# Kernel tuning notes

Hardware: AMD Instinct MI355X
Metric: run time of the kernel (lower is better)

## Reference

```python
import jax, jax.numpy as jnp
import numpy as np
import math


def setup_inputs() -> dict:
    key = jax.random.key(0)
    ks = jax.random.split(key, 5)
    B, C, E = 4, 2048, 1024
    max_len = 2048
    s = 1.0 / math.sqrt(E)
    return {
        "x": jax.random.normal(ks[0], (B, C, E), dtype=jnp.float32),
        "W_q": jax.random.normal(ks[1], (E, E), dtype=jnp.float32) * s,
        "W_k": jax.random.normal(ks[2], (E, E), dtype=jnp.float32) * s,
        "W_v": jax.random.normal(ks[3], (E, E), dtype=jnp.float32) * s,
        "rel_bias": jax.random.normal(ks[4], (2 * max_len - 1, 1), dtype=jnp.float32),
        "max_len": max_len,
    }


def reference(x, W_q, W_k, W_v, rel_bias, max_len):
    B, C, E = x.shape
    # nn.Linear(bias=False): y = x @ W.T
    Q = jnp.einsum("bce,fe->bcf", x, W_q)
    K = jnp.einsum("bce,fe->bcf", x, W_k)
    V = jnp.einsum("bce,fe->bcf", x, W_v)
    scores = jnp.einsum("bqe,bke->bqk", Q, K) / math.sqrt(E)
    pos = jnp.arange(C)
    rel_dist = jnp.clip(pos[None, :] - pos[:, None] + (max_len - 1), 0, 2 * max_len - 2)
    bias = rel_bias[rel_dist, 0]  # [C, C]
    scores = scores + bias[None, :, :]
    weights = jax.nn.softmax(scores, axis=-1)
    out = jnp.einsum("bqk,bke->bqe", weights, V)
    return out, weights
```

## Files before the change

kernel.cpp:

```cpp
#include <hip/hip_runtime.h>
#include <hip/hip_bf16.h>
#include <math.h>

typedef __attribute__((ext_vector_type(8))) short short8;
typedef __attribute__((ext_vector_type(4))) short short4v;
typedef __attribute__((ext_vector_type(4))) float f32x4;

static __device__ __forceinline__ short f2bf(float f) {
  union { float f; unsigned u; } x;
  x.f = f;
  unsigned r = x.u + 0x7fffu + ((x.u >> 16) & 1u);
  return (short)(r >> 16);
}

#define GLD16(g, l)                                                   \
  __builtin_amdgcn_global_load_lds(                                   \
      (const __attribute__((address_space(1))) void*)(g),             \
      (__attribute__((address_space(3))) void*)(l), 16, 0, 0)
#define BAR() asm volatile("s_barrier" ::: "memory")
#define VMCNT6() asm volatile("s_waitcnt vmcnt(6)" ::: "memory")
#define VMCNT0() asm volatile("s_waitcnt vmcnt(0)" ::: "memory")

__global__ __launch_bounds__(256) void cvt_all(
    const float* __restrict__ x, const float* __restrict__ wq,
    const float* __restrict__ wk, const float* __restrict__ wv,
    short* __restrict__ xb, short* __restrict__ wqb,
    short* __restrict__ wkb, short* __restrict__ wvb, int n0, int n1) {
  int i = blockIdx.x * 256 + threadIdx.x;
  const float* src; short* dst; int off;
  if (i < n0) { src = x; dst = xb; off = i; }
  else if (i < n0 + n1) { src = wq; dst = wqb; off = i - n0; }
  else if (i < n0 + 2 * n1) { src = wk; dst = wkb; off = i - n0 - n1; }
  else if (i < n0 + 3 * n1) { src = wv; dst = wvb; off = i - n0 - 2 * n1; }
  else return;
  const float4* p = (const float4*)src + (size_t)off * 2;
  float4 a = p[0], b = p[1];
  short8 o;
  o[0] = f2bf(a.x); o[1] = f2bf(a.y); o[2] = f2bf(a.z); o[3] = f2bf(a.w);
  o[4] = f2bf(b.x); o[5] = f2bf(b.y); o[6] = f2bf(b.z); o[7] = f2bf(b.w);
  *((short8*)dst + off) = o;
}

template <int MODE>
__global__ __launch_bounds__(256, 2) void gemm_wt(
    const short* __restrict__ A, const short* __restrict__ Bt,
    void* __restrict__ C0, void* __restrict__ C1, void* __restrict__ C2,
    const float* __restrict__ rel_bias,
    int N, int K, long aZ, long bZ, long cZ, int Cdim, float scale, int ml) {
  __shared__ short sA[3][256 * 32];
  __shared__ short sB[3][128 * 32];
  const int tid = threadIdx.x, lane = tid & 63, wid = tid >> 6;

  const int gx = gridDim.x, gy = gridDim.y;
  const int nwg = gx * gy * (int)gridDim.z;
  const int f = ((int)blockIdx.z * gy + (int)blockIdx.y) * gx + (int)blockIdx.x;
  const int qq = nwg >> 3, rr = nwg & 7;
  const int xcd = f & 7, pos = f >> 3;
  const int lg = (xcd < rr ? xcd * (qq + 1) : rr * (qq + 1) + (xcd - rr) * qq) + pos;
  const int z = lg / (gx * gy);
  const int rem = lg - z * (gx * gy);
  const int bx = rem / gy, by = rem - bx * gy;

  const short* Az = A + (size_t)z * aZ;
  const short* Bz = Bt + (size_t)z * bZ;
  const int brow = bx * 256, bcol = by * 128;
  const int lrow = lane & 15, kg = lane >> 4;

  const int t4 = tid >> 2;
  const int logslot = (tid & 3) ^ ((tid >> 3) & 3);
  const short* aSrc[4];
#pragma unroll
  for (int c = 0; c < 4; ++c)
    aSrc[c] = Az + (size_t)(brow + c * 64 + t4) * K + logslot * 8;
  const short* bSrc[2];
#pragma unroll
  for (int c = 0; c < 2; ++c)
    bSrc[c] = Bz + (size_t)(bcol + c * 64 + t4) * K + logslot * 8;
  const int dW = wid * 512;

  const int kOff = (kg ^ ((lrow >> 1) & 3)) * 8;
  const int aBase = (wid * 64 + lrow) * 32 + kOff;
  const int bBase = lrow * 32 + kOff;

  short8 a[4], b[8];
  f32x4 acc[4][8] = {};

  short *pa0 = &sA[0][0], *pa1 = &sA[1][0], *pa2 = &sA[2][0];
  short *pb0 = &sB[0][0], *pb1 = &sB[1][0], *pb2 = &sB[2][0];

#define STG(PA, PB, T)                                               \
  do {                                                               \
    GLD16(aSrc[0] + (size_t)(T) * 32, (PA) + 0 * 2048 + dW);         \
    GLD16(aSrc[1] + (size_t)(T) * 32, (PA) + 1 * 2048 + dW);         \
    GLD16(aSrc[2] + (size_t)(T) * 32, (PA) + 2 * 2048 + dW);         \
    GLD16(aSrc[3] + (size_t)(T) * 32, (PA) + 3 * 2048 + dW);         \
    GLD16(bSrc[0] + (size_t)(T) * 32, (PB) + 0 * 2048 + dW);         \
    GLD16(bSrc[1] + (size_t)(T) * 32, (PB) + 1 * 2048 + dW);         \
  } while (0)
#define RD(PA, PB)                                                  \
  do {                                                              \
    _Pragma("unroll") for (int m = 0; m < 4; ++m)                   \
        a[m] = *(const short8*)&(PA)[aBase + m * 512];              \
    _Pragma("unroll") for (int n = 0; n < 8; ++n)                   \
        b[n] = *(const short8*)&(PB)[bBase + n * 512];              \
  } while (0)
#define MFMA32()                                                              \
  do {                                                                        \
    __builtin_amdgcn_s_setprio(1);                                            \
    _Pragma("unroll") for (int m = 0; m < 4; ++m)                             \
        _Pragma("unroll") for (int n = 0; n < 8; ++n)                         \
            acc[m][n] = __builtin_amdgcn_mfma_f32_16x16x32_bf16(              \
                a[m], b[n], acc[m][n], 0, 0, 0);                              \
    __builtin_amdgcn_s_setprio(0);                                            \
  } while (0)
#define ROT()                                                    \
  do {                                                           \
    short* q;                                                    \
    q = pa0; pa0 = pa1; pa1 = pa2; pa2 = q;                      \
    q = pb0; pb0 = pb1; pb1 = pb2; pb2 = q;                      \
  } while (0)

  STG(pa0, pb0, 0);
  STG(pa1, pb1, 1);

  const int NT = K >> 5;
  for (int t = 0; t < NT - 2; ++t) {
    VMCNT6();
    BAR();
    RD(pa0, pb0);
    STG(pa2, pb2, t + 2);
    MFMA32();
    ROT();
  }
  VMCNT6();
  BAR();
  RD(pa0, pb0);
  MFMA32();
  ROT();
  VMCNT0();
  BAR();
  RD(pa0, pb0);
  MFMA32();

#pragma unroll
  for (int m = 0; m < 4; ++m) {
#pragma unroll
    for (int n = 0; n < 8; ++n) {
#pragma unroll
      for (int r = 0; r < 4; ++r) {
        float v = acc[m][n][r];
        int gr = brow + wid * 64 + m * 16 + kg * 4 + r;
        int gc = bcol + n * 16 + lrow;
        if constexpr (MODE == 2) {
          int idx = gc - gr + (ml - 1);
          idx = min(max(idx, 0), 2 * ml - 2);
          ((float*)C0 + (size_t)z * cZ)[(size_t)gr * N + gc] =
              v * scale + rel_bias[idx];
        } else if constexpr (MODE == 3) {
          ((float*)C0 + (size_t)z * cZ)[(size_t)gr * N + gc] = v;
        } else {
          int s = gc >> 10, cc = gc & 1023;
          short* dst = (s == 0) ? (short*)C0 : (s == 1) ? (short*)C1 : (short*)C2;
          dst[(size_t)gr * 1024 + cc] = f2bf(v);
        }
      }
    }
  }
#undef STG
#undef RD
#undef MFMA32
#undef ROT
}

__global__ __launch_bounds__(256) void transpose_v(const short* __restrict__ vin,
                                                   short* __restrict__ vout,
                                                   int Cd, int E) {
  __shared__ short t[64][72];
  const int c0 = blockIdx.x * 64, e0 = blockIdx.y * 64, b = blockIdx.z;
  const int tid = threadIdx.x;
  const int cr = tid >> 2;
  const int ec = (tid & 3) * 16;
  const short* src = vin + ((size_t)b * Cd + c0 + cr) * E + e0 + ec;
  short8 v0 = *(const short8*)src;
  short8 v1 = *(const short8*)(src + 8);
#pragma unroll
  for (int j = 0; j < 8; ++j) t[ec + j][cr] = v0[j];
#pragma unroll
  for (int j = 0; j < 8; ++j) t[ec + 8 + j][cr] = v1[j];
  __syncthreads();
  const int er = tid >> 2;
  const int cc = (tid & 3) * 16;
  short* dst = vout + ((size_t)b * E + e0 + er) * Cd + c0 + cc;
  *(short8*)dst = *(const short8*)&t[er][cc];
  *(short8*)(dst + 8) = *(const short8*)&t[er][cc + 8];
}

__global__ __launch_bounds__(256) void softmax_rows(float* __restrict__ w,
                                                    short* __restrict__ wb, int Cd) {
  const size_t row = blockIdx.x;
  float4* p = (float4*)(w + row * (size_t)Cd);
  const int tid = threadIdx.x;
  float4 v0 = p[tid];
  float4 v1 = p[tid + 256];
  float mx = fmaxf(fmaxf(fmaxf(v0.x, v0.y), fmaxf(v0.z, v0.w)),
                   fmaxf(fmaxf(v1.x, v1.y), fmaxf(v1.z, v1.w)));
#pragma unroll
  for (int o = 32; o; o >>= 1) mx = fmaxf(mx, __shfl_xor(mx, o));
  __shared__ float red[8];
  const int wv = tid >> 6;
  if ((tid & 63) == 0) red[wv] = mx;
  __syncthreads();
  mx = fmaxf(fmaxf(red[0], red[1]), fmaxf(red[2], red[3]));
  v0.x = __expf(v0.x - mx); v0.y = __expf(v0.y - mx);
  v0.z = __expf(v0.z - mx); v0.w = __expf(v0.w - mx);
  v1.x = __expf(v1.x - mx); v1.y = __expf(v1.y - mx);
  v1.z = __expf(v1.z - mx); v1.w = __expf(v1.w - mx);
  float s = v0.x + v0.y + v0.z + v0.w + v1.x + v1.y + v1.z + v1.w;
#pragma unroll
  for (int o = 32; o; o >>= 1) s += __shfl_xor(s, o);
  if ((tid & 63) == 0) red[4 + wv] = s;
  __syncthreads();
  s = red[4] + red[5] + red[6] + red[7];
  float inv = 1.0f / s;
  v0.x *= inv; v0.y *= inv; v0.z *= inv; v0.w *= inv;
  v1.x *= inv; v1.y *= inv; v1.z *= inv; v1.w *= inv;
  p[tid] = v0;
  p[tid + 256] = v1;
  short4v b0, b1;
  b0[0] = f2bf(v0.x); b0[1] = f2bf(v0.y); b0[2] = f2bf(v0.z); b0[3] = f2bf(v0.w);
  b1[0] = f2bf(v1.x); b1[1] = f2bf(v1.y); b1[2] = f2bf(v1.z); b1[3] = f2bf(v1.w);
  short* wrow = wb + row * (size_t)Cd;
  *(short4v*)&wrow[tid * 4] = b0;
  *(short4v*)&wrow[1024 + tid * 4] = b1;
}

extern "C" void kernel_launch(void* const* d_in, const int* in_sizes, int n_in,
                              void* d_out, int out_size, void* d_ws, size_t ws_size,
                              hipStream_t stream) {
  const float* x = (const float*)d_in[0];
  const float* Wq = (const float*)d_in[1];
  const float* Wk = (const float*)d_in[2];
  const float* Wv = (const float*)d_in[3];
  const float* rb = (const float*)d_in[4];

  const int E = 1024;
  const int Mt = in_sizes[0] / E;
  const int Cd = out_size / Mt - E;
  const int B = Mt / Cd;
  const int ml = (in_sizes[4] + 1) / 2;
  const float scale = 1.0f / sqrtf((float)E);

  short* xb = (short*)d_ws;
  short* wqb = xb + (size_t)Mt * E;
  short* wkb = wqb + (size_t)E * E;
  short* wvb = wkb + (size_t)E * E;
  short* Qb = wvb + (size_t)E * E;
  short* Kb = Qb + (size_t)Mt * E;
  short* Vrow = Kb + (size_t)Mt * E;
  short* Vt = xb;
  short* wbf = Qb;

  float* outp = (float*)d_out;
  float* wts = outp + (size_t)Mt * E;

  const int n0 = (Mt * E) / 8, n1 = (E * E) / 8;
  cvt_all<<<(n0 + 3 * n1 + 255) / 256, 256, 0, stream>>>(
      x, Wq, Wk, Wv, xb, wqb, wkb, wvb, n0, n1);

  dim3 blk(256);
  gemm_wt<4><<<dim3(Mt / 256, 3 * E / 128, 1), blk, 0, stream>>>(
      xb, wqb, Qb, Kb, Vrow, nullptr, 3 * E, E, 0, 0, 0, Cd, 0.f, ml);
  gemm_wt<2><<<dim3(Cd / 256, Cd / 128, B), blk, 0, stream>>>(
      Qb, Kb, wts, nullptr, nullptr, rb, Cd, E, (long)Cd * E, (long)Cd * E,
      (long)Cd * Cd, Cd, scale, ml);
  softmax_rows<<<Mt, 256, 0, stream>>>(wts, wbf, Cd);
  transpose_v<<<dim3(Cd / 64, E / 64, B), 256, 0, stream>>>(Vrow, Vt, Cd, E);
  gemm_wt<3><<<dim3(Cd / 256, E / 128, B), blk, 0, stream>>>(
      wbf, Vt, outp, nullptr, nullptr, nullptr, E, Cd, (long)Cd * Cd,
      (long)E * Cd, (long)Cd * E, Cd, 0.f, ml);
}
```

Baseline: 193.8 us.

## Unroll GEMM k-loop by three with static LDS buffers and narrower PV tile

```diff
diff --git a/kernel.cpp b/kernel.cpp
--- a/kernel.cpp
+++ b/kernel.cpp
@@ -18,8 +18,7 @@
       (const __attribute__((address_space(1))) void*)(g),             \
       (__attribute__((address_space(3))) void*)(l), 16, 0, 0)
 #define BAR() asm volatile("s_barrier" ::: "memory")
-#define VMCNT6() asm volatile("s_waitcnt vmcnt(6)" ::: "memory")
-#define VMCNT0() asm volatile("s_waitcnt vmcnt(0)" ::: "memory")
+#define VM0() asm volatile("s_waitcnt vmcnt(0)" ::: "memory")
 
 __global__ __launch_bounds__(256) void cvt_all(
     const float* __restrict__ x, const float* __restrict__ wq,
@@ -41,14 +40,16 @@
   *((short8*)dst + off) = o;
 }
 
-template <int MODE>
-__global__ __launch_bounds__(256, 2) void gemm_wt(
+template <int MODE, int BN>
+__global__ __launch_bounds__(256, 2) void gemm_u3(
     const short* __restrict__ A, const short* __restrict__ Bt,
     void* __restrict__ C0, void* __restrict__ C1, void* __restrict__ C2,
     const float* __restrict__ rel_bias,
     int N, int K, long aZ, long bZ, long cZ, int Cdim, float scale, int ml) {
+  constexpr int NREP = BN / 16;
+  constexpr int BCH = BN / 64;
   __shared__ short sA[3][256 * 32];
-  __shared__ short sB[3][128 * 32];
+  __shared__ short sB[3][BN * 32];
   const int tid = threadIdx.x, lane = tid & 63, wid = tid >> 6;
 
   const int gx = gridDim.x, gy = gridDim.y;
@@ -63,89 +64,119 @@
 
   const short* Az = A + (size_t)z * aZ;
   const short* Bz = Bt + (size_t)z * bZ;
-  const int brow = bx * 256, bcol = by * 128;
+  const int brow = bx * 256, bcol = by * BN;
   const int lrow = lane & 15, kg = lane >> 4;
 
   const int t4 = tid >> 2;
   const int logslot = (tid & 3) ^ ((tid >> 3) & 3);
-  const short* aSrc[4];
+  const short* aS[4];
 #pragma unroll
   for (int c = 0; c < 4; ++c)
-    aSrc[c] = Az + (size_t)(brow + c * 64 + t4) * K + logslot * 8;
-  const short* bSrc[2];
-#pragma unroll
-  for (int c = 0; c < 2; ++c)
-    bSrc[c] = Bz + (size_t)(bcol + c * 64 + t4) * K + logslot * 8;
+    aS[c] = Az + (size_t)(brow + c * 64 + t4) * K + logslot * 8;
+  const short* bS[BCH];
+#pragma unroll
+  for (int c = 0; c < BCH; ++c)
+    bS[c] = Bz + (size_t)(bcol + c * 64 + t4) * K + logslot * 8;
   const int dW = wid * 512;
 
   const int kOff = (kg ^ ((lrow >> 1) & 3)) * 8;
   const int aBase = (wid * 64 + lrow) * 32 + kOff;
   const int bBase = lrow * 32 + kOff;
 
-  short8 a[4], b[8];
-  f32x4 acc[4][8] = {};
-
-  short *pa0 = &sA[0][0], *pa1 = &sA[1][0], *pa2 = &sA[2][0];
-  short *pb0 = &sB[0][0], *pb1 = &sB[1][0], *pb2 = &sB[2][0];
-
-#define STG(PA, PB, T)                                               \
+  short8 a[4], b[NREP];
+  f32x4 acc[4][NREP] = {};
+
+  short* const pa0 = &sA[0][0];
+  short* const pa1 = &sA[1][0];
+  short* const pa2 = &sA[2][0];
+  short* const pb0 = &sB[0][0];
+  short* const pb1 = &sB[1][0];
+  short* const pb2 = &sB[2][0];
+
+#define STG(PA, PB, OFF)                                             \
   do {                                                               \
-    GLD16(aSrc[0] + (size_t)(T) * 32, (PA) + 0 * 2048 + dW);         \
-    GLD16(aSrc[1] + (size_t)(T) * 32, (PA) + 1 * 2048 + dW);         \
-    GLD16(aSrc[2] + (size_t)(T) * 32, (PA) + 2 * 2048 + dW);         \
-    GLD16(aSrc[3] + (size_t)(T) * 32, (PA) + 3 * 2048 + dW);         \
-    GLD16(bSrc[0] + (size_t)(T) * 32, (PB) + 0 * 2048 + dW);         \
-    GLD16(bSrc[1] + (size_t)(T) * 32, (PB) + 1 * 2048 + dW);         \
+    GLD16(aS[0] + (OFF), (PA) + 0 * 2048 + dW);                      \
+    GLD16(aS[1] + (OFF), (PA) + 1 * 2048 + dW);                      \
+    GLD16(aS[2] + (OFF), (PA) + 2 * 2048 + dW);                      \
+    GLD16(aS[3] + (OFF), (PA) + 3 * 2048 + dW);                      \
+    GLD16(bS[0] + (OFF), (PB) + 0 * 2048 + dW);                      \
+    if constexpr (BCH == 2) GLD16(bS[1] + (OFF), (PB) + 2048 + dW);  \
   } while (0)
 #define RD(PA, PB)                                                  \
   do {                                                              \
     _Pragma("unroll") for (int m = 0; m < 4; ++m)                   \
         a[m] = *(const short8*)&(PA)[aBase + m * 512];              \
-    _Pragma("unroll") for (int n = 0; n < 8; ++n)                   \
+    _Pragma("unroll") for (int n = 0; n < NREP; ++n)                \
         b[n] = *(const short8*)&(PB)[bBase + n * 512];              \
   } while (0)
-#define MFMA32()                                                              \
+#define MFMA_ALL()                                                            \
   do {                                                                        \
     __builtin_amdgcn_s_setprio(1);                                            \
     _Pragma("unroll") for (int m = 0; m < 4; ++m)                             \
-        _Pragma("unroll") for (int n = 0; n < 8; ++n)                         \
+        _Pragma("unroll") for (int n = 0; n < NREP; ++n)                      \
             acc[m][n] = __builtin_amdgcn_mfma_f32_16x16x32_bf16(              \
                 a[m], b[n], acc[m][n], 0, 0, 0);                              \
     __builtin_amdgcn_s_setprio(0);                                            \
   } while (0)
-#define ROT()                                                    \
-  do {                                                           \
-    short* q;                                                    \
-    q = pa0; pa0 = pa1; pa1 = pa2; pa2 = q;                      \
-    q = pb0; pb0 = pb1; pb1 = pb2; pb2 = q;                      \
+#define VM_LPT()                                                    \
+  do {                                                              \
+    if constexpr (BCH == 2)                                         \
+      asm volatile("s_waitcnt vmcnt(6)" ::: "memory");              \
+    else                                                            \
+      asm volatile("s_waitcnt vmcnt(5)" ::: "memory");              \
   } while (0)
 
   STG(pa0, pb0, 0);
-  STG(pa1, pb1, 1);
+  STG(pa1, pb1, 32);
 
   const int NT = K >> 5;
-  for (int t = 0; t < NT - 2; ++t) {
-    VMCNT6();
-    BAR();
+  const int G = (NT - 2) / 3;
+  for (int g = 0; g < G; ++g) {
+    VM_LPT(); BAR();
     RD(pa0, pb0);
-    STG(pa2, pb2, t + 2);
-    MFMA32();
-    ROT();
+    STG(pa2, pb2, 64);
+    MFMA_ALL();
+    VM_LPT(); BAR();
+    RD(pa1, pb1);
+    STG(pa0, pb0, 96);
+    MFMA_ALL();
+    VM_LPT(); BAR();
+    RD(pa2, pb2);
+    STG(pa1, pb1, 128);
+    MFMA_ALL();
+#pragma unroll
+    for (int c = 0; c < 4; ++c) aS[c] += 96;
+#pragma unroll
+    for (int c = 0; c < BCH; ++c) bS[c] += 96;
   }
-  VMCNT6();
-  BAR();
-  RD(pa0, pb0);
-  MFMA32();
-  ROT();
-  VMCNT0();
-  BAR();
-  RD(pa0, pb0);
-  MFMA32();
+  if ((NT - 2) % 3 == 2) {
+    VM_LPT(); BAR();
+    RD(pa0, pb0);
+    STG(pa2, pb2, 64);
+    MFMA_ALL();
+    VM_LPT(); BAR();
+    RD(pa1, pb1);
+    STG(pa0, pb0, 96);
+    MFMA_ALL();
+    VM_LPT(); BAR();
+    RD(pa2, pb2);
+    MFMA_ALL();
+    VM0(); BAR();
+    RD(pa0, pb0);
+    MFMA_ALL();
+  } else {
+    VM_LPT(); BAR();
+    RD(pa0, pb0);
+    MFMA_ALL();
+    VM0(); BAR();
+    RD(pa1, pb1);
+    MFMA_ALL();
+  }
 
 #pragma unroll
   for (int m = 0; m < 4; ++m) {
 #pragma unroll
-    for (int n = 0; n < 8; ++n) {
+    for (int n = 0; n < NREP; ++n) {
 #pragma unroll
       for (int r = 0; r < 4; ++r) {
         float v = acc[m][n][r];
@@ -168,8 +199,8 @@
   }
 #undef STG
 #undef RD
-#undef MFMA32
-#undef ROT
+#undef MFMA_ALL
+#undef VM_LPT
 }
 
 __global__ __launch_bounds__(256) void transpose_v(const short* __restrict__ vin,
@@ -268,14 +299,14 @@
       x, Wq, Wk, Wv, xb, wqb, wkb, wvb, n0, n1);
 
   dim3 blk(256);
-  gemm_wt<4><<<dim3(Mt / 256, 3 * E / 128, 1), blk, 0, stream>>>(
+  gemm_u3<4, 128><<<dim3(Mt / 256, 3 * E / 128, 1), blk, 0, stream>>>(
       xb, wqb, Qb, Kb, Vrow, nullptr, 3 * E, E, 0, 0, 0, Cd, 0.f, ml);
-  gemm_wt<2><<<dim3(Cd / 256, Cd / 128, B), blk, 0, stream>>>(
+  gemm_u3<2, 128><<<dim3(Cd / 256, Cd / 128, B), blk, 0, stream>>>(
       Qb, Kb, wts, nullptr, nullptr, rb, Cd, E, (long)Cd * E, (long)Cd * E,
       (long)Cd * Cd, Cd, scale, ml);
   softmax_rows<<<Mt, 256, 0, stream>>>(wts, wbf, Cd);
   transpose_v<<<dim3(Cd / 64, E / 64, B), 256, 0, stream>>>(Vrow, Vt, Cd, E);
-  gemm_wt<3><<<dim3(Cd / 256, E / 128, B), blk, 0, stream>>>(
+  gemm_u3<3, 64><<<dim3(Cd / 256, E / 64, B), blk, 0, stream>>>(
       wbf, Vt, outp, nullptr, nullptr, nullptr, E, Cd, (long)Cd * Cd,
       (long)E * Cd, (long)Cd * E, Cd, 0.f, ml);
 }
```

New measurement: 248.0 us. 28.0% more time.
